# Performance work log

Measured on AMD Instinct MI355X. Metric: run time of the kernel, lower is better.

## Reference

```python
import jax, jax.numpy as jnp
import numpy as np

N_NODES = 100000
N_EDGES = 800000
IN_DIM, HID_DIM, OUT_DIM = 128, 256, 40


def setup_inputs() -> dict:
    key = jax.random.key(0)
    ks = jax.random.split(key, 8)
    x = jax.random.normal(ks[0], (N_NODES, IN_DIM), dtype=jnp.float32)
    edge_index = jax.random.randint(ks[1], (2, N_EDGES), 0, N_NODES, dtype=jnp.int64)
    # PyG SAGEConv params: lin_l (neighbor path, with bias), lin_r (root path, no bias)
    def glorot(k, fan_in, fan_out):
        lim = np.sqrt(6.0 / (fan_in + fan_out)).astype(np.float32)
        return jax.random.uniform(k, (fan_in, fan_out), jnp.float32, -lim, lim)
    W1l = glorot(ks[2], IN_DIM, HID_DIM)
    W1r = glorot(ks[3], IN_DIM, HID_DIM)
    b1 = jnp.zeros((HID_DIM,), jnp.float32)
    W2l = glorot(ks[4], HID_DIM, OUT_DIM)
    W2r = glorot(ks[5], HID_DIM, OUT_DIM)
    b2 = jnp.zeros((OUT_DIM,), jnp.float32)
    return {"x": x, "edge_index": edge_index, "W1l": W1l, "b1": b1, "W1r": W1r,
            "W2l": W2l, "b2": b2, "W2r": W2r}


def _sage_conv(x, src, dst, Wl, b, Wr, n_nodes):
    # mean aggregation of neighbor features: gather x[src], scatter-add to dst, divide by degree
    msg = x[src]                                              # [E, D]
    agg = jax.ops.segment_sum(msg, dst, num_segments=n_nodes)  # [N, D]
    cnt = jax.ops.segment_sum(jnp.ones((src.shape[0],), x.dtype), dst,
                              num_segments=n_nodes)            # [N]
    agg = agg / jnp.maximum(cnt, 1.0)[:, None]
    # out = lin_l(mean_agg) + lin_r(x)  (lin_l carries the bias in PyG)
    return agg @ Wl + b + x @ Wr


def reference(x, edge_index, W1l, b1, W1r, W2l, b2, W2r):
    src, dst = edge_index[0], edge_index[1]
    n = x.shape[0]
    h = _sage_conv(x, src, dst, W1l, b1, W1r, n)
    h = jax.nn.relu(h)
    # F.dropout(training=self.training): identity at inference
    out = _sage_conv(h, src, dst, W2l, b2, W2r, n)
    return out
```

## Files before the change

### kernel.cpp

```cpp
#include <hip/hip_runtime.h>
#include <hip/hip_bf16.h>


#define NN   100000
#define NNP  100096
#define NE   800000
#define NB1  391

typedef unsigned short ushortT;
typedef __attribute__((ext_vector_type(8))) short bf16x8;
typedef __attribute__((ext_vector_type(4))) float f32x4;

__device__ __forceinline__ unsigned short f2b(float f) {
    unsigned u = __float_as_uint(f);
    return (unsigned short)((u + 0x7fffu + ((u >> 16) & 1u)) >> 16);
}
__device__ __forceinline__ float b2f(unsigned short v) {
    return __uint_as_float(((unsigned)v) << 16);
}
__device__ __forceinline__ void llds16(const unsigned short* g, unsigned short* s) {
    __builtin_amdgcn_global_load_lds(
        (const __attribute__((address_space(1))) void*)g,
        (__attribute__((address_space(3))) void*)s, 16, 0, 0);
}

__global__ __launch_bounds__(256) void k_prep_rank(
        const float* __restrict__ x,
        const float* __restrict__ W1l, const float* __restrict__ W1r,
        const float* __restrict__ W2l, const float* __restrict__ W2r,
        ushortT* __restrict__ Ac, ushortT* __restrict__ WT1,
        ushortT* __restrict__ WT2,
        const int* __restrict__ dst, int* __restrict__ deg8,
        int* __restrict__ rank) {
    int bid = blockIdx.x;
    if (bid < 12500) {
        int t = bid * 256 + threadIdx.x;
        int row = t >> 5, c4 = t & 31;
        float4 v = *(const float4*)&x[(size_t)row * 128 + c4 * 4];
        ushortT* p = Ac + (size_t)row * 256 + 128 + c4 * 4;
        p[0] = f2b(v.x); p[1] = f2b(v.y); p[2] = f2b(v.z); p[3] = f2b(v.w);

        if (t < 65536) {
            int n = t >> 8, k = t & 255;
            float w = (k < 128) ? W1l[(size_t)k * 256 + n]
                                : W1r[(size_t)(k - 128) * 256 + n];
            WT1[t] = f2b(w);
        } else if (t < 65536 + 20480) {
            int j = t - 65536;
            int n = j >> 8, k = j & 255;
            float w = (n < 40) ? W2l[(size_t)k * 40 + n]
                               : W2r[(size_t)k * 40 + (n - 40)];
            WT2[j] = f2b(w);
        }
    } else {
        int idx = bid - 12500;
        int e = idx * 256 + threadIdx.x;
        int r = idx & 7;
        rank[e] = atomicAdd(&deg8[r * NN + dst[e]], 1);
    }
}

__global__ __launch_bounds__(256) void k_scan1(const int* __restrict__ deg8,
                                               int* __restrict__ rp,
                                               int* __restrict__ rpp,
                                               int* __restrict__ bsum) {
    __shared__ int s[256];
    int t = threadIdx.x;
    int i = blockIdx.x * 256 + t;
    int d8[8];
    int v = 0;
#pragma unroll
    for (int r = 0; r < 8; ++r) {
        d8[r] = (i < NN) ? deg8[r * NN + i] : 0;
        v += d8[r];
    }
    s[t] = v;
    __syncthreads();
    for (int off = 1; off < 256; off <<= 1) {
        int add = (t >= off) ? s[t - off] : 0;
        __syncthreads();
        s[t] += add;
        __syncthreads();
    }
    int ex = s[t] - v;
    if (i <= NN) rp[i] = ex;
    if (i < NN) {
        int run = ex;
#pragma unroll
        for (int r = 0; r < 8; ++r) {
            rpp[r * NN + i] = run;
            run += d8[r];
        }
    }
    if (t == 255) bsum[blockIdx.x] = s[255];
}

__global__ __launch_bounds__(512) void k_scan2(int* __restrict__ bsum) {
    __shared__ int s[512];
    int t = threadIdx.x;
    int v = (t < NB1) ? bsum[t] : 0;
    s[t] = v;
    __syncthreads();
    for (int off = 1; off < 512; off <<= 1) {
        int add = (t >= off) ? s[t - off] : 0;
        __syncthreads();
        s[t] += add;
        __syncthreads();
    }
    if (t < NB1) bsum[t] = s[t] - v;
}

__global__ __launch_bounds__(256) void k_fill(const int* __restrict__ src,
                                              const int* __restrict__ dst,
                                              const int* __restrict__ rank,
                                              const int* __restrict__ rpp,
                                              const int* __restrict__ bsum,
                                              int* __restrict__ col) {
    int fbid = blockIdx.x;
    int chunk = fbid >> 3;
    int lo = (fbid & 7) * 12500, hi = lo + 12500;
    int base = chunk * 2048 + threadIdx.x;
#pragma unroll
    for (int j = 0; j < 8; ++j) {
        int e = base + j * 256;
        if (e < NE) {
            int d = dst[e];
            if (d >= lo && d < hi) {
                int r = (e >> 8) & 7;
                col[bsum[d >> 8] + rpp[r * NN + d] + rank[e]] = src[e];
            }
        }
    }
}

__global__ __launch_bounds__(256) void k_agg1(const int* __restrict__ rp,
                                              const int* __restrict__ bsum,
                                              const int* __restrict__ col,
                                              ushortT* __restrict__ Ac) {
    int node = blockIdx.x * 4 + (threadIdx.x >> 6);
    int l = threadIdx.x & 63;
    if (node >= NN) return;
    int seg = l >> 4, dl = l & 15;
    int beg = rp[node] + bsum[node >> 8];
    int end = rp[node + 1] + bsum[(node + 1) >> 8];
    int deg = end - beg;
    float a[8] = {0.f, 0.f, 0.f, 0.f, 0.f, 0.f, 0.f, 0.f};
    for (int base = 0; base < deg; base += 64) {
        int cnt = min(64, deg - base);
        int cv = col[beg + base + min(l, cnt - 1)];
        for (int j = 0; j < cnt; j += 8) {
            int e0 = j + seg, e1 = j + 4 + seg;
            int i0 = __shfl(cv, min(e0, cnt - 1));
            int i1 = __shfl(cv, min(e1, cnt - 1));
            bf16x8 v0 = {0, 0, 0, 0, 0, 0, 0, 0};
            bf16x8 v1 = {0, 0, 0, 0, 0, 0, 0, 0};
            if (e0 < cnt) v0 = *(const bf16x8*)(Ac + (size_t)i0 * 256 + 128 + dl * 8);
            if (e1 < cnt) v1 = *(const bf16x8*)(Ac + (size_t)i1 * 256 + 128 + dl * 8);
#pragma unroll
            for (int i = 0; i < 8; ++i)
                a[i] += b2f((unsigned short)v0[i]) + b2f((unsigned short)v1[i]);
        }
    }
#pragma unroll
    for (int i = 0; i < 8; ++i) {
        a[i] += __shfl_xor(a[i], 16);
        a[i] += __shfl_xor(a[i], 32);
    }
    if (seg == 0) {
        float inv = 1.0f / fmaxf((float)deg, 1.0f);
        bf16x8 o;
#pragma unroll
        for (int i = 0; i < 8; ++i) o[i] = (short)f2b(a[i] * inv);
        *(bf16x8*)(Ac + (size_t)node * 256 + dl * 8) = o;
    }
}

#define HSP 264
__global__ __launch_bounds__(256, 3) void k_fused(
        const ushortT* __restrict__ Ac, const ushortT* __restrict__ WT1,
        const float* __restrict__ b1, const ushortT* __restrict__ WT2,
        const float* __restrict__ b2, ushortT* __restrict__ y2,
        ushortT* __restrict__ t) {
    __shared__ ushortT As[64 * 64];
    __shared__ ushortT Bs[64 * HSP];
    const int tid = threadIdx.x, l = tid & 63, wid = tid >> 6;
    const int m0 = blockIdx.x * 64;
    const int q = l >> 4, r = l & 15;
    const int swz = (l & 7) ^ ((l >> 3) & 7);

    f32x4 acc[4][4];
#pragma unroll
    for (int i = 0; i < 4; ++i)
#pragma unroll
        for (int j = 0; j < 4; ++j) acc[i][j] = (f32x4){0.f, 0.f, 0.f, 0.f};

    for (int kt = 0; kt < 256; kt += 64) {
#pragma unroll
        for (int i = 0; i < 2; ++i) {
            int flat = wid * 2 + i;
            int row = flat * 8 + (l >> 3);
            llds16(Ac + (size_t)(m0 + row) * 256 + kt + swz * 8, &As[flat * 512]);
        }
#pragma unroll
        for (int i = 0; i < 8; ++i) {
            int flat = wid * 8 + i;
            int row = flat * 8 + (l >> 3);
            llds16(WT1 + (size_t)row * 256 + kt + swz * 8, &Bs[flat * 512]);
        }
        __syncthreads();
#pragma unroll
        for (int ks = 0; ks < 64; ks += 32) {
            bf16x8 af[4], bfr[4];
            const int cs = (((ks >> 3) + q) ^ (r & 7)) * 8;
#pragma unroll
            for (int mt = 0; mt < 4; ++mt)
                af[mt] = *(const bf16x8*)&As[(mt * 16 + r) * 64 + cs];
#pragma unroll
            for (int nt = 0; nt < 4; ++nt)
                bfr[nt] = *(const bf16x8*)&Bs[(wid * 64 + nt * 16 + r) * 64 + cs];
#pragma unroll
            for (int mt = 0; mt < 4; ++mt)
#pragma unroll
                for (int nt = 0; nt < 4; ++nt)
                    acc[mt][nt] = __builtin_amdgcn_mfma_f32_16x16x32_bf16(
                        af[mt], bfr[nt], acc[mt][nt], 0, 0, 0);
        }
        __syncthreads();
    }
#pragma unroll
    for (int nt = 0; nt < 4; ++nt) {
        int colb = wid * 64 + nt * 16 + r;
        float bb = b1[colb];
#pragma unroll
        for (int mt = 0; mt < 4; ++mt) {
            int rowb = mt * 16 + q * 4;
#pragma unroll
            for (int j = 0; j < 4; ++j)
                Bs[(rowb + j) * HSP + colb] = f2b(fmaxf(acc[mt][nt][j] + bb, 0.f));
        }
    }
    __syncthreads();

    f32x4 acc2[2][4];
#pragma unroll
    for (int i = 0; i < 2; ++i)
#pragma unroll
        for (int j = 0; j < 4; ++j) acc2[i][j] = (f32x4){0.f, 0.f, 0.f, 0.f};
#pragma unroll
    for (int kk = 0; kk < 256; kk += 32) {
        bf16x8 af[4];
#pragma unroll
        for (int mt = 0; mt < 4; ++mt)
            af[mt] = *(const bf16x8*)&Bs[(mt * 16 + r) * HSP + kk + q * 8];
#pragma unroll
        for (int cc = 0; cc < 2; ++cc) {
            int ct = wid + cc * 4;
            if (ct < 5) {
                bf16x8 bq = *(const bf16x8*)(WT2 + (size_t)(ct * 16 + r) * 256 + kk + q * 8);
#pragma unroll
                for (int mt = 0; mt < 4; ++mt)
                    acc2[cc][mt] = __builtin_amdgcn_mfma_f32_16x16x32_bf16(
                        af[mt], bq, acc2[cc][mt], 0, 0, 0);
            }
        }
    }
#pragma unroll
    for (int cc = 0; cc < 2; ++cc) {
        int ct = wid + cc * 4;
        if (ct >= 5) continue;
        int c = ct * 16 + r;
        float bb = (c >= 40) ? b2[c - 40] : 0.f;
#pragma unroll
        for (int mt = 0; mt < 4; ++mt) {
            int row0 = m0 + mt * 16 + q * 4;
#pragma unroll
            for (int j = 0; j < 4; ++j) {
                float v = acc2[cc][mt][j];
                if (c < 40)
                    y2[(size_t)(row0 + j) * 40 + c] = f2b(v);
                else
                    t[(size_t)(row0 + j) * 40 + (c - 40)] = f2b(v + bb);
            }
        }
    }
}

__global__ __launch_bounds__(256) void k_agg2(const int* __restrict__ rp,
                                              const int* __restrict__ bsum,
                                              const int* __restrict__ col,
                                              const ushortT* __restrict__ y2,
                                              const ushortT* __restrict__ t,
                                              float* __restrict__ out) {
    int node = blockIdx.x * 4 + (threadIdx.x >> 6);
    int l = threadIdx.x & 63;
    if (node >= NN) return;
    int seg = l >> 4, dl = l & 15;
    int beg = rp[node] + bsum[node >> 8];
    int end = rp[node + 1] + bsum[(node + 1) >> 8];
    int deg = end - beg;
    bool act = dl < 10;
    float a0 = 0.f, a1 = 0.f, a2 = 0.f, a3 = 0.f;
    for (int base = 0; base < deg; base += 64) {
        int cnt = min(64, deg - base);
        int cv = col[beg + base + min(l, cnt - 1)];
        for (int j = 0; j < cnt; j += 8) {
            int e0 = j + seg, e1 = j + 4 + seg;
            int i0 = __shfl(cv, min(e0, cnt - 1));
            int i1 = __shfl(cv, min(e1, cnt - 1));
            ushort4 v0 = {0, 0, 0, 0}, v1 = {0, 0, 0, 0};
            if (e0 < cnt && act) v0 = *(const ushort4*)(y2 + (size_t)i0 * 40 + dl * 4);
            if (e1 < cnt && act) v1 = *(const ushort4*)(y2 + (size_t)i1 * 40 + dl * 4);
            a0 += b2f(v0.x) + b2f(v1.x);
            a1 += b2f(v0.y) + b2f(v1.y);
            a2 += b2f(v0.z) + b2f(v1.z);
            a3 += b2f(v0.w) + b2f(v1.w);
        }
    }
    a0 += __shfl_xor(a0, 16); a0 += __shfl_xor(a0, 32);
    a1 += __shfl_xor(a1, 16); a1 += __shfl_xor(a1, 32);
    a2 += __shfl_xor(a2, 16); a2 += __shfl_xor(a2, 32);
    a3 += __shfl_xor(a3, 16); a3 += __shfl_xor(a3, 32);
    if (seg == 0 && act) {
        float inv = 1.0f / fmaxf((float)deg, 1.0f);
        size_t o = (size_t)node * 40 + dl * 4;
        ushort4 tv = *(const ushort4*)&t[o];
        float4 ov;
        ov.x = a0 * inv + b2f(tv.x);
        ov.y = a1 * inv + b2f(tv.y);
        ov.z = a2 * inv + b2f(tv.z);
        ov.w = a3 * inv + b2f(tv.w);
        *(float4*)&out[o] = ov;
    }
}

extern "C" void kernel_launch(void* const* d_in, const int* in_sizes, int n_in,
                              void* d_out, int out_size, void* d_ws, size_t ws_size,
                              hipStream_t stream) {
    const float* x   = (const float*)d_in[0];
    const int*   ei  = (const int*)d_in[1];
    const int*   src = ei;
    const int*   dst = ei + NE;
    const float* W1l = (const float*)d_in[2];
    const float* b1  = (const float*)d_in[3];
    const float* W1r = (const float*)d_in[4];
    const float* W2l = (const float*)d_in[5];
    const float* b2  = (const float*)d_in[6];
    const float* W2r = (const float*)d_in[7];
    float* out = (float*)d_out;

    size_t off = 0;
    char* base = (char*)d_ws;
    auto alloc = [&](size_t bytes) -> void* {
        void* p = base + off;
        off += (bytes + 255) & ~(size_t)255;
        return p;
    };
    int*     deg8  = (int*)alloc((size_t)8 * NN * 4);
    int*     rp    = (int*)alloc((size_t)(NN + 1) * 4);
    int*     rpp   = (int*)alloc((size_t)8 * NN * 4);
    int*     rank  = (int*)alloc((size_t)NE * 4);
    int*     col   = (int*)alloc((size_t)NE * 4);
    int*     bsum  = (int*)alloc(512 * 4);
    ushortT* Ac    = (ushortT*)alloc((size_t)NNP * 256 * 2);
    ushortT* y2    = (ushortT*)alloc((size_t)NNP * 40 * 2);
    ushortT* t     = (ushortT*)alloc((size_t)NNP * 40 * 2);
    ushortT* WT1   = (ushortT*)alloc(256 * 256 * 2);
    ushortT* WT2   = (ushortT*)alloc(80 * 256 * 2);

    hipMemsetAsync(deg8, 0, (size_t)8 * NN * 4, stream);
    k_prep_rank<<<15625, 256, 0, stream>>>(x, W1l, W1r, W2l, W2r, Ac, WT1, WT2,
                                           dst, deg8, rank);
    k_scan1<<<NB1, 256, 0, stream>>>(deg8, rp, rpp, bsum);
    k_scan2<<<1, 512, 0, stream>>>(bsum);
    k_fill<<<391 * 8, 256, 0, stream>>>(src, dst, rank, rpp, bsum, col);
    k_agg1<<<(NN + 3) / 4, 256, 0, stream>>>(rp, bsum, col, Ac);
    k_fused<<<NNP / 64, 256, 0, stream>>>(Ac, WT1, b1, WT2, b2, y2, t);
    k_agg2<<<(NN + 3) / 4, 256, 0, stream>>>(rp, bsum, col, y2, t, out);
}
```

Baseline: 271.7 us.

## Build CSR with per-slice LDS histograms instead of global atomics and rank array

```diff
diff --git a/kernel.cpp b/kernel.cpp
--- a/kernel.cpp
+++ b/kernel.cpp
@@ -6,6 +6,8 @@
 #define NNP  100096
 #define NE   800000
 #define NB1  391
+#define NSL  3125
+#define NCH  100000
 
 typedef unsigned short ushortT;
 typedef __attribute__((ext_vector_type(8))) short bf16x8;
@@ -24,14 +26,14 @@
         (__attribute__((address_space(3))) void*)s, 16, 0, 0);
 }
 
-__global__ __launch_bounds__(256) void k_prep_rank(
+__global__ __launch_bounds__(256) void k_prep(
         const float* __restrict__ x,
         const float* __restrict__ W1l, const float* __restrict__ W1r,
         const float* __restrict__ W2l, const float* __restrict__ W2r,
         ushortT* __restrict__ Ac, ushortT* __restrict__ WT1,
         ushortT* __restrict__ WT2,
-        const int* __restrict__ dst, int* __restrict__ deg8,
-        int* __restrict__ rank) {
+        const int* __restrict__ dst, int* __restrict__ deg8) {
+    __shared__ int hist[NSL];
     int bid = blockIdx.x;
     if (bid < 12500) {
         int t = bid * 256 + threadIdx.x;
@@ -54,9 +56,17 @@
         }
     } else {
         int idx = bid - 12500;
-        int e = idx * 256 + threadIdx.x;
-        int r = idx & 7;
-        rank[e] = atomicAdd(&deg8[r * NN + dst[e]], 1);
+        int c = idx & 7, s = idx >> 3;
+        for (int i = threadIdx.x; i < NSL; i += 256) hist[i] = 0;
+        __syncthreads();
+        int e0 = c * NCH, lo = s * NSL;
+        for (int i = threadIdx.x; i < NCH; i += 256) {
+            unsigned dd = (unsigned)(dst[e0 + i] - lo);
+            if (dd < (unsigned)NSL) atomicAdd(&hist[dd], 1);
+        }
+        __syncthreads();
+        for (int i = threadIdx.x; i < NSL; i += 256)
+            deg8[c * NN + lo + i] = hist[i];
     }
 }
 
@@ -110,25 +120,23 @@
     if (t < NB1) bsum[t] = s[t] - v;
 }
 
-__global__ __launch_bounds__(256) void k_fill(const int* __restrict__ src,
-                                              const int* __restrict__ dst,
-                                              const int* __restrict__ rank,
-                                              const int* __restrict__ rpp,
-                                              const int* __restrict__ bsum,
-                                              int* __restrict__ col) {
-    int fbid = blockIdx.x;
-    int chunk = fbid >> 3;
-    int lo = (fbid & 7) * 12500, hi = lo + 12500;
-    int base = chunk * 2048 + threadIdx.x;
-#pragma unroll
-    for (int j = 0; j < 8; ++j) {
-        int e = base + j * 256;
-        if (e < NE) {
-            int d = dst[e];
-            if (d >= lo && d < hi) {
-                int r = (e >> 8) & 7;
-                col[bsum[d >> 8] + rpp[r * NN + d] + rank[e]] = src[e];
-            }
+__global__ __launch_bounds__(256) void k_fillcsr(const int* __restrict__ src,
+                                                 const int* __restrict__ dst,
+                                                 const int* __restrict__ rpp,
+                                                 const int* __restrict__ bsum,
+                                                 int* __restrict__ col) {
+    __shared__ int hist[NSL];
+    int s = blockIdx.x & 31, c = blockIdx.x >> 5;
+    for (int i = threadIdx.x; i < NSL; i += 256) hist[i] = 0;
+    __syncthreads();
+    int e0 = c * NCH, lo = s * NSL;
+    for (int i = threadIdx.x; i < NCH; i += 256) {
+        int e = e0 + i;
+        int d = dst[e];
+        unsigned dd = (unsigned)(d - lo);
+        if (dd < (unsigned)NSL) {
+            int k = atomicAdd(&hist[dd], 1);
+            col[bsum[d >> 8] + rpp[c * NN + d] + k] = src[e];
         }
     }
 }
@@ -358,7 +366,6 @@
     int*     deg8  = (int*)alloc((size_t)8 * NN * 4);
     int*     rp    = (int*)alloc((size_t)(NN + 1) * 4);
     int*     rpp   = (int*)alloc((size_t)8 * NN * 4);
-    int*     rank  = (int*)alloc((size_t)NE * 4);
     int*     col   = (int*)alloc((size_t)NE * 4);
     int*     bsum  = (int*)alloc(512 * 4);
     ushortT* Ac    = (ushortT*)alloc((size_t)NNP * 256 * 2);
@@ -367,12 +374,11 @@
     ushortT* WT1   = (ushortT*)alloc(256 * 256 * 2);
     ushortT* WT2   = (ushortT*)alloc(80 * 256 * 2);
 
-    hipMemsetAsync(deg8, 0, (size_t)8 * NN * 4, stream);
-    k_prep_rank<<<15625, 256, 0, stream>>>(x, W1l, W1r, W2l, W2r, Ac, WT1, WT2,
-                                           dst, deg8, rank);
+    k_prep<<<12756, 256, 0, stream>>>(x, W1l, W1r, W2l, W2r, Ac, WT1, WT2,
+                                      dst, deg8);
     k_scan1<<<NB1, 256, 0, stream>>>(deg8, rp, rpp, bsum);
     k_scan2<<<1, 512, 0, stream>>>(bsum);
-    k_fill<<<391 * 8, 256, 0, stream>>>(src, dst, rank, rpp, bsum, col);
+    k_fillcsr<<<256, 256, 0, stream>>>(src, dst, rpp, bsum, col);
     k_agg1<<<(NN + 3) / 4, 256, 0, stream>>>(rp, bsum, col, Ac);
     k_fused<<<NNP / 64, 256, 0, stream>>>(Ac, WT1, b1, WT2, b2, y2, t);
     k_agg2<<<(NN + 3) / 4, 256, 0, stream>>>(rp, bsum, col, y2, t, out);
```

After: 508.9 us. 1.87x slower.
